# Kernel optimization log

Hardware: AMD Instinct MI355X
Metric: run time of the kernel (lower is better)

Reference implementation:

```python
import jax, jax.numpy as jnp
import numpy as np

PS = 16          # patch_size
E = 256          # embed_dim
NH = 4           # num_heads
THR = 1.5        # entropy_threshold (bits)
LN_EPS = 1e-5


def _ln(x, g, b):
    m = x.mean(-1, keepdims=True)
    v = ((x - m) ** 2).mean(-1, keepdims=True)
    return (x - m) / jnp.sqrt(v + LN_EPS) * g + b


def _forward(video, conv_w, conv_b, wq_w, wq_b, wk_w, wk_b, wv_w, wv_b,
             lnq_g, lnq_b, lnk_g, lnk_b, lnv_g, lnv_b,
             in_proj_w, in_proj_b, out_proj_w, out_proj_b,
             dense_w, dense_b, bproj_w, bproj_b, group_query, ent_table):
    # Conv3d(3->E, k=(3,PS,PS), s=(2,PS,PS), p=(1,0,0)) + ReLU
    x = jax.lax.conv_general_dilated(
        video, conv_w, window_strides=(2, PS, PS),
        padding=((1, 1), (0, 0), (0, 0)),
        dimension_numbers=('NCDHW', 'OIDHW', 'NCDHW'))
    x = jax.nn.relu(x + conv_b[None, :, None, None, None])
    B = x.shape[0]
    tokens = x.reshape(B, E, -1).transpose(0, 2, 1)  # [B, N, E]
    N = tokens.shape[1]

    # per-token byte (no_grad in torch)
    byte = jax.lax.stop_gradient(
        jnp.clip(jnp.round(tokens.mean(-1) * 255.0), 0, 255)).astype(jnp.int32)  # [B, N]
    # entropy predictor: probs = softmax(ent_table[last_byte]) (last byte of running seq)
    logits = ent_table[byte[0]]                      # [N, 256]
    p = jax.nn.softmax(logits, axis=-1)
    ent = -(p * jnp.log2(p + 1e-9)).sum(-1)          # [N]
    boundary = (ent > THR).astype(jnp.int32)
    seg = jnp.cumsum(boundary) - boundary            # exclusive cumsum -> segment id per token

    # DecoderCrossAttention with a single shared group_query per segment
    q0 = jnp.broadcast_to(group_query, (B, 1, E))    # byte_representations
    query = _ln(q0 @ wq_w.T + wq_b, lnq_g, lnq_b)    # [B,1,E]
    k = _ln(tokens @ wk_w.T + wk_b, lnk_g, lnk_b)    # [B,N,E]
    v = _ln(tokens @ wv_w.T + wv_b, lnv_g, lnv_b)

    Wqi, Wki, Wvi = in_proj_w[:E], in_proj_w[E:2 * E], in_proj_w[2 * E:]
    bqi, bki, bvi = in_proj_b[:E], in_proj_b[E:2 * E], in_proj_b[2 * E:]
    dh = E // NH
    qp = ((query @ Wqi.T + bqi) * (dh ** -0.5)).reshape(B, NH, dh)  # [B,H,dh]
    kp = (k @ Wki.T + bki).reshape(B, N, NH, dh)
    vp = (v @ Wvi.T + bvi).reshape(B, N, NH, dh)

    scores = jnp.einsum('bhd,bnhd->nbh', qp, kp)     # [N,B,H]
    smax = jax.ops.segment_max(scores, seg, num_segments=N)   # [N,B,H]
    w = jnp.exp(scores - smax[seg])
    denom = jax.ops.segment_sum(w, seg, num_segments=N)       # [N,B,H]
    num = jax.ops.segment_sum(w[..., None] * vp.transpose(1, 0, 2, 3),
                              seg, num_segments=N)            # [N,B,H,dh]
    count = jax.ops.segment_sum(jnp.ones((N,), scores.dtype), seg, num_segments=N)
    valid = count > 0
    safe = jnp.where(valid[:, None, None], denom, 1.0)
    attn = (num / safe[..., None]).transpose(1, 0, 2, 3).reshape(B, N, E)
    out = attn @ out_proj_w.T + out_proj_b
    out = out @ dense_w.T + dense_b
    out = out + q0                                   # residual with byte_representations
    patches = out @ bproj_w.T + bproj_b              # binary_proj
    return jnp.where(valid[None, :, None], patches, 0.0)  # [B, N, E] padded


def setup_inputs() -> dict:
    key = jax.random.key(0)
    ks = jax.random.split(key, 16)
    rn = lambda k, s, sc=0.02: jax.random.normal(k, s, jnp.float32) * sc
    z = lambda *s: jnp.zeros(s, jnp.float32)
    o = lambda *s: jnp.ones(s, jnp.float32)
    return {
        'video': jax.random.normal(ks[0], (4, 3, 32, 224, 224), jnp.float32),
        'conv_w': rn(ks[1], (E, 3, 3, PS, PS)), 'conv_b': z(E),
        'wq_w': rn(ks[2], (E, E)), 'wq_b': z(E),
        'wk_w': rn(ks[3], (E, E)), 'wk_b': z(E),
        'wv_w': rn(ks[4], (E, E)), 'wv_b': z(E),
        'lnq_g': o(E), 'lnq_b': z(E),
        'lnk_g': o(E), 'lnk_b': z(E),
        'lnv_g': o(E), 'lnv_b': z(E),
        'in_proj_w': rn(ks[5], (3 * E, E)), 'in_proj_b': z(3 * E),
        'out_proj_w': rn(ks[6], (E, E)), 'out_proj_b': z(E),
        'dense_w': rn(ks[7], (E, E)), 'dense_b': z(E),
        'bproj_w': rn(ks[8], (E, E)), 'bproj_b': z(E),
        'group_query': jax.random.normal(ks[9], (1, 1, E), jnp.float32),
        'ent_table': jax.random.normal(ks[10], (256, 256), jnp.float32) * 6.0,
    }


def reference(video, conv_w, conv_b, wq_w, wq_b, wk_w, wk_b, wv_w, wv_b,
              lnq_g, lnq_b, lnk_g, lnk_b, lnv_g, lnv_b,
              in_proj_w, in_proj_b, out_proj_w, out_proj_b,
              dense_w, dense_b, bproj_w, bproj_b, group_query, ent_table):
    return _forward(video, conv_w, conv_b, wq_w, wq_b, wk_w, wk_b, wv_w, wv_b,
                    lnq_g, lnq_b, lnk_g, lnk_b, lnv_g, lnv_b,
                    in_proj_w, in_proj_b, out_proj_w, out_proj_b,
                    dense_w, dense_b, bproj_w, bproj_b, group_query, ent_table)
```

## Files before the change

kernel.cpp:

```cpp
#include <hip/hip_runtime.h>
#include <hip/hip_bf16.h>
#include <math.h>

#define NTOK 3136
#define MT 12544
#define KCV 2304
#define THRESH 1.5f
#define LN_EPS 1e-5f

typedef short short8 __attribute__((ext_vector_type(8)));
typedef float f32x4 __attribute__((ext_vector_type(4)));
typedef float f32x16 __attribute__((ext_vector_type(16)));

__device__ __forceinline__ unsigned short f2bf(float f) {
    unsigned int u = __float_as_uint(f);
    u += 0x7fffu + ((u >> 16) & 1u);
    return (unsigned short)(u >> 16);
}
__device__ __forceinline__ float bf2f(unsigned short h) {
    return __uint_as_float(((unsigned int)h) << 16);
}
__device__ __forceinline__ unsigned int cvt_pk_bf16(float x0, float x1) {
    union { __hip_bfloat162 h; unsigned int u; } cv;
    cv.h = __float22bfloat162_rn(make_float2(x0, x1));
    return cv.u;
}
__device__ __forceinline__ void async16(const void* g, void* l) {
    __builtin_amdgcn_global_load_lds((const __attribute__((address_space(1))) void*)g,
                                     (__attribute__((address_space(3))) void*)l, 16, 0, 0);
}

__device__ __forceinline__ float wsum(float v) {
#pragma unroll
    for (int o = 32; o > 0; o >>= 1) v += __shfl_xor(v, o);
    return v;
}
__device__ __forceinline__ float wmax(float v) {
#pragma unroll
    for (int o = 32; o > 0; o >>= 1) v = fmaxf(v, __shfl_xor(v, o));
    return v;
}

__global__ __launch_bounds__(256) void prep_k(
    const float* __restrict__ cw, unsigned short* __restrict__ cwh,
    unsigned short* __restrict__ cwl,
    const float* __restrict__ s0, const float* __restrict__ s1, const float* __restrict__ s2,
    const float* __restrict__ s3, const float* __restrict__ s4, const float* __restrict__ s5,
    unsigned short* __restrict__ dst,
    const float* __restrict__ gq, const float* __restrict__ wq_w,
    const float* __restrict__ wq_b, const float* __restrict__ lnq_g,
    const float* __restrict__ lnq_b, const float* __restrict__ inW,
    const float* __restrict__ inB, float* __restrict__ qp)
{
    const int blk = blockIdx.x;
    if (blk < 288) {
        int i = blk * 256 + threadIdx.x;
        int e = i & 255, kg = i >> 8;
        const float4* sp = (const float4*)(cw + (size_t)e * KCV + kg * 8);
        float4 x0 = sp[0], x1 = sp[1];
        float av[8] = {x0.x, x0.y, x0.z, x0.w, x1.x, x1.y, x1.z, x1.w};
        short8 hh, ll;
#pragma unroll
        for (int j = 0; j < 8; ++j) {
            unsigned short h = f2bf(av[j]);
            hh[j] = (short)h;
            ll[j] = (short)f2bf(av[j] - bf2f(h));
        }
        size_t off = (size_t)kg * 2048 + e * 8;
        *(short8*)&cwh[off] = hh;
        *(short8*)&cwl[off] = ll;
    } else if (blk < 2336) {
        int i = (blk - 288) * 256 + threadIdx.x;
        if (i >= 524288) return;
        float v;
        if      (i <  65536) v = s0[i];
        else if (i < 131072) v = s1[i - 65536];
        else if (i < 327680) v = s2[i - 131072];
        else if (i < 393216) v = s3[i - 327680];
        else if (i < 458752) v = s4[i - 393216];
        else                 v = s5[i - 458752];
        dst[i] = f2bf(v);
    } else {
        __shared__ float sh[256];
        __shared__ float red[256];
        const int t = threadIdx.x;
        float acc = wq_b[t];
        for (int j = 0; j < 256; j++) acc += gq[j] * wq_w[t * 256 + j];
        red[t] = acc; __syncthreads();
        for (int o = 128; o > 0; o >>= 1) { if (t < o) red[t] += red[t + o]; __syncthreads(); }
        float m = red[0] * (1.f / 256.f);
        __syncthreads();
        float d = acc - m;
        red[t] = d * d; __syncthreads();
        for (int o = 128; o > 0; o >>= 1) { if (t < o) red[t] += red[t + o]; __syncthreads(); }
        float inv = 1.f / sqrtf(red[0] * (1.f / 256.f) + LN_EPS);
        sh[t] = d * inv * lnq_g[t] + lnq_b[t];
        __syncthreads();
        float a2 = inB[t];
        for (int j = 0; j < 256; j++) a2 += sh[j] * inW[t * 256 + j];
        qp[t] = a2 * 0.125f;
    }
}

__global__ __launch_bounds__(256, 3) void conv_mfma_k(
    const float* __restrict__ video, const unsigned short* __restrict__ cwh,
    const unsigned short* __restrict__ cwl, const float* __restrict__ cbias,
    float* __restrict__ tokmean8, unsigned short* __restrict__ outB)
{
    __shared__ __align__(16) unsigned short Bh[8192], Bl[8192];
    const int t    = threadIdx.x;
    const int lane = t & 63;
    const int w    = t >> 6;
    const int l31  = lane & 31, lh = lane >> 5;
    const int wr   = w >> 1,    wc = w & 1;
    const int v_  = blockIdx.x;
    const int s_  = (v_ & 7) * 98 + (v_ >> 3);
    const int mb  = s_ >> 2, eb = s_ & 3;
    const int m0  = mb * 64, e0 = eb * 64;

    const int m = m0 + wr * 32 + l31;
    const int b = m / NTOK, n = m % NTOK;
    const int d = n / 196, hw = n % 196;
    const int h = hw / 14, ww = hw % 14;
    const float* vb = video + (size_t)(b * 3) * (32 * 50176) + (h * 16) * 224 + ww * 16;
    const int dbase = 2 * d - 1;

    f32x16 acc = {};
    float4 a0, a1, a2, a3, a4, a5, a6, a7;
    float4 n0, n1, n2, n3, n4, n5, n6, n7;
    short8 rh0, rh1, rl0, rl1;

#define BLOAD(s)                                                                     \
    {                                                                                \
        const size_t g0 = (size_t)((s) * 8 + (t >> 5)) * 2048 + (e0 + (t & 31) * 2) * 8; \
        rh0 = *(const short8*)(cwh + g0);                                            \
        rh1 = *(const short8*)(cwh + g0 + 8);                                        \
        rl0 = *(const short8*)(cwl + g0);                                            \
        rl1 = *(const short8*)(cwl + g0 + 8);                                        \
    }
#define BSTORE(buf)                                                                  \
    {                                                                                \
        const int o = (buf) * 4096 + (t >> 5) * 512 + (t & 31) * 16;                 \
        *(short8*)&Bh[o]     = rh0;                                                  \
        *(short8*)&Bh[o + 8] = rh1;                                                  \
        *(short8*)&Bl[o]     = rl0;                                                  \
        *(short8*)&Bl[o + 8] = rl1;                                                  \
    }
#define LOAD_OCT(kv, x0, x1)                                                         \
    {                                                                                \
        const int k0  = (kv) + lh * 8;                                               \
        const int c   = k0 / 768;                                                    \
        const int rem = k0 - c * 768;                                                \
        const int kd  = rem >> 8;                                                    \
        const int r2  = rem & 255;                                                   \
        const int id  = dbase + kd;                                                  \
        x0 = make_float4(0.f, 0.f, 0.f, 0.f); x1 = x0;                               \
        if (id >= 0) {                                                               \
            const float* p = vb + (size_t)c * (32 * 50176) + id * 50176 +            \
                             (r2 >> 4) * 224 + (r2 & 15);                            \
            x0 = *(const float4*)p;                                                  \
            x1 = *(const float4*)(p + 4);                                            \
        }                                                                            \
    }
#define CVT_AB(y0, y1, fah, fal)                                                     \
    short8 fah, fal;                                                                 \
    {                                                                                \
        float av[8] = {y0.x, y0.y, y0.z, y0.w, y1.x, y1.y, y1.z, y1.w};              \
        unsigned int ph[4], pl[4];                                                   \
        _Pragma("unroll")                                                            \
        for (int j = 0; j < 4; ++j) {                                                \
            float u0 = av[2 * j], u1 = av[2 * j + 1];                                \
            unsigned int hu = cvt_pk_bf16(u0, u1);                                   \
            float r0 = u0 - __uint_as_float(hu << 16);                               \
            float r1 = u1 - __uint_as_float(hu & 0xffff0000u);                       \
            ph[j] = hu;                                                              \
            pl[j] = cvt_pk_bf16(r0, r1);                                             \
        }                                                                            \
        int4 phv = make_int4(ph[0], ph[1], ph[2], ph[3]);                            \
        int4 plv = make_int4(pl[0], pl[1], pl[2], pl[3]);                            \
        fah = *(short8*)&phv;                                                        \
        fal = *(short8*)&plv;                                                        \
    }
#define KCHUNK(i, ya, yb, cbuf)                                                      \
    {                                                                                \
        CVT_AB(ya, yb, fah, fal);                                                    \
        const int rb = (cbuf) * 4096 + ((2 * (i) + lh) * 64 + wc * 32 + l31) * 8;    \
        short8 fbh = *(const short8*)&Bh[rb];                                        \
        short8 fbl = *(const short8*)&Bl[rb];                                        \
        acc = __builtin_amdgcn_mfma_f32_32x32x16_bf16(fah, fbh, acc, 0, 0, 0);       \
        acc = __builtin_amdgcn_mfma_f32_32x32x16_bf16(fah, fbl, acc, 0, 0, 0);       \
        acc = __builtin_amdgcn_mfma_f32_32x32x16_bf16(fal, fbh, acc, 0, 0, 0);       \
    }

    BLOAD(0);
    LOAD_OCT(0,  a0, a1);
    LOAD_OCT(16, a2, a3);
    LOAD_OCT(32, a4, a5);
    LOAD_OCT(48, a6, a7);
    BSTORE(0);
    __syncthreads();

    for (int s = 0; s < 36; ++s) {
        const int cbuf = s & 1;
        if (s + 1 < 36) {
            BLOAD(s + 1);
            const int kb = (s + 1) * 64;
            LOAD_OCT(kb,      n0, n1);
            LOAD_OCT(kb + 16, n2, n3);
            LOAD_OCT(kb + 32, n4, n5);
            LOAD_OCT(kb + 48, n6, n7);
        }
        KCHUNK(0, a0, a1, cbuf);
        KCHUNK(1, a2, a3, cbuf);
        KCHUNK(2, a4, a5, cbuf);
        KCHUNK(3, a6, a7, cbuf);
        if (s + 1 < 36) BSTORE(cbuf ^ 1);
        __syncthreads();
        a0 = n0; a1 = n1; a2 = n2; a3 = n3;
        a4 = n4; a5 = n5; a6 = n6; a7 = n7;
    }
#undef BLOAD
#undef BSTORE
#undef LOAD_OCT
#undef CVT_AB
#undef KCHUNK

    const int e = e0 + wc * 32 + l31;
    const float bias = cbias[e];
    const bool emit_tm = (m0 < NTOK);
#pragma unroll
    for (int r = 0; r < 16; ++r) {
        int row = (r & 3) + 8 * (r >> 2) + 4 * lh;
        int mm  = m0 + wr * 32 + row;
        float vv = fmaxf(acc[r] + bias, 0.f);
        outB[(size_t)mm * 256 + e] = f2bf(vv);
        float sv = vv;
        sv += __shfl_xor(sv, 1); sv += __shfl_xor(sv, 2);
        sv += __shfl_xor(sv, 4); sv += __shfl_xor(sv, 8);
        sv += __shfl_xor(sv, 16);
        if (emit_tm && l31 == 0)
            tokmean8[(size_t)(eb * 2 + wc) * NTOK + mm] = sv;
    }
}

__global__ __launch_bounds__(256) void gemm_single_k(
    const unsigned short* __restrict__ A, const unsigned short* __restrict__ W,
    const float* __restrict__ bias, const float* __restrict__ addvec,
    const int* __restrict__ Sptr, float* __restrict__ outF, unsigned short* __restrict__ outB)
{
    __shared__ __align__(16) unsigned short As[8192], Bs[8192];
    const int t = threadIdx.x, lane = t & 63, w = t >> 6;
    const int v_ = blockIdx.x;
    const int s_ = (v_ & 7) * 98 + (v_ >> 3);
    const int m0 = (s_ >> 2) * 64, e0 = (s_ & 3) * 64;
    const int l15 = lane & 15, lq = lane >> 4;
    const unsigned short* ga = A + (size_t)(m0 + lane) * 256;
    const unsigned short* gb = W + (size_t)(e0 + lane) * 256;
#pragma unroll
    for (int kg = w; kg < 16; kg += 4) {
        async16(ga + kg * 8, &As[kg * 512]);
        async16(gb + kg * 8, &Bs[kg * 512]);
    }
    f32x4 acc[4] = {};
    __syncthreads();
#pragma unroll
    for (int s = 0; s < 4; ++s) {
        int kg = s * 4 + lq;
        short8 a = *(const short8*)&As[kg * 512 + (w * 16 + l15) * 8];
#pragma unroll
        for (int ct = 0; ct < 4; ++ct) {
            short8 bb = *(const short8*)&Bs[kg * 512 + (ct * 16 + l15) * 8];
            acc[ct] = __builtin_amdgcn_mfma_f32_16x16x32_bf16(a, bb, acc[ct], 0, 0, 0);
        }
    }
    __syncthreads();
#pragma unroll
    for (int kg = w; kg < 16; kg += 4) {
        async16(ga + (16 + kg) * 8, &As[kg * 512]);
        async16(gb + (16 + kg) * 8, &Bs[kg * 512]);
    }
    __syncthreads();
#pragma unroll
    for (int s = 0; s < 4; ++s) {
        int kg = s * 4 + lq;
        short8 a = *(const short8*)&As[kg * 512 + (w * 16 + l15) * 8];
#pragma unroll
        for (int ct = 0; ct < 4; ++ct) {
            short8 bb = *(const short8*)&Bs[kg * 512 + (ct * 16 + l15) * 8];
            acc[ct] = __builtin_amdgcn_mfma_f32_16x16x32_bf16(a, bb, acc[ct], 0, 0, 0);
        }
    }
    int S = Sptr ? *Sptr : 0x7fffffff;
    int rbase = m0 + w * 16 + lq * 4;
#pragma unroll
    for (int ct = 0; ct < 4; ++ct) {
        int e = e0 + ct * 16 + l15;
        float bv = bias[e] + (addvec ? addvec[e] : 0.f);
#pragma unroll
        for (int r = 0; r < 4; ++r) {
            int mm = rbase + r;
            float vv = acc[ct][r] + bv;
            if ((mm % NTOK) >= S) vv = 0.f;
            size_t off = (size_t)mm * 256 + e;
            if (outF) outF[off] = vv;
            if (outB) outB[off] = f2bf(vv);
        }
    }
}

__global__ __launch_bounds__(256) void gemm_dual_k(
    const unsigned short* __restrict__ A0, const unsigned short* __restrict__ A1,
    const unsigned short* __restrict__ W,
    const float* __restrict__ bias0, const float* __restrict__ bias1,
    unsigned short* __restrict__ outB0, unsigned short* __restrict__ outB1,
    const float* __restrict__ qp, float* __restrict__ sc)
{
    __shared__ __align__(16) unsigned short As[8192], Bs[8192];
    const int t = threadIdx.x, lane = t & 63, w = t >> 6;
    const int v_ = blockIdx.x;
    const int s_ = (v_ & 7) * 196 + (v_ >> 3);
    const int mb = s_ >> 3, ebg = s_ & 7;
    const int half = ebg >> 2;
    const unsigned short* A = half ? A1 : A0;
    const float* bias = half ? bias1 : bias0;
    unsigned short* outB = half ? outB1 : outB0;
    const int m0 = mb * 64, eg0 = ebg * 64, el0 = (ebg & 3) * 64;
    const int l15 = lane & 15, lq = lane >> 4;
    const unsigned short* ga = A + (size_t)(m0 + lane) * 256;
    const unsigned short* gb = W + (size_t)(eg0 + lane) * 256;
#pragma unroll
    for (int kg = w; kg < 16; kg += 4) {
        async16(ga + kg * 8, &As[kg * 512]);
        async16(gb + kg * 8, &Bs[kg * 512]);
    }
    f32x4 acc[4] = {};
    __syncthreads();
#pragma unroll
    for (int s = 0; s < 4; ++s) {
        int kg = s * 4 + lq;
        short8 a = *(const short8*)&As[kg * 512 + (w * 16 + l15) * 8];
#pragma unroll
        for (int ct = 0; ct < 4; ++ct) {
            short8 bb = *(const short8*)&Bs[kg * 512 + (ct * 16 + l15) * 8];
            acc[ct] = __builtin_amdgcn_mfma_f32_16x16x32_bf16(a, bb, acc[ct], 0, 0, 0);
        }
    }
    __syncthreads();
#pragma unroll
    for (int kg = w; kg < 16; kg += 4) {
        async16(ga + (16 + kg) * 8, &As[kg * 512]);
        async16(gb + (16 + kg) * 8, &Bs[kg * 512]);
    }
    __syncthreads();
#pragma unroll
    for (int s = 0; s < 4; ++s) {
        int kg = s * 4 + lq;
        short8 a = *(const short8*)&As[kg * 512 + (w * 16 + l15) * 8];
#pragma unroll
        for (int ct = 0; ct < 4; ++ct) {
            short8 bb = *(const short8*)&Bs[kg * 512 + (ct * 16 + l15) * 8];
            acc[ct] = __builtin_amdgcn_mfma_f32_16x16x32_bf16(a, bb, acc[ct], 0, 0, 0);
        }
    }
    int rbase = m0 + w * 16 + lq * 4;
    if (qp && half == 0) {
        float sp[4] = {0.f, 0.f, 0.f, 0.f};
#pragma unroll
        for (int ct = 0; ct < 4; ++ct) {
            int e = el0 + ct * 16 + l15;
            float bv = bias[e];
            float qv = qp[e];
#pragma unroll
            for (int r = 0; r < 4; ++r) sp[r] += (acc[ct][r] + bv) * qv;
        }
#pragma unroll
        for (int r = 0; r < 4; ++r) {
            sp[r] += __shfl_xor(sp[r], 1); sp[r] += __shfl_xor(sp[r], 2);
            sp[r] += __shfl_xor(sp[r], 4); sp[r] += __shfl_xor(sp[r], 8);
        }
        if (l15 == 0) {
#pragma unroll
            for (int r = 0; r < 4; ++r) {
                int mm = rbase + r;
                int bb = mm / NTOK, nn = mm % NTOK;
                sc[(bb * 4 + ebg) * NTOK + nn] = sp[r];
            }
        }
    } else {
#pragma unroll
        for (int ct = 0; ct < 4; ++ct) {
            int e = el0 + ct * 16 + l15;
            float bv = bias[e];
#pragma unroll
            for (int r = 0; r < 4; ++r) {
                float vv = acc[ct][r] + bv;
                outB[(size_t)(rbase + r) * 256 + e] = f2bf(vv);
            }
        }
    }
}

__global__ __launch_bounds__(256) void boundary_k(
    const float* __restrict__ tokmean8, const float* __restrict__ ent_table,
    int* __restrict__ boundary)
{
    int n    = blockIdx.x * 4 + (threadIdx.x >> 6);
    int lane = threadIdx.x & 63;
    float s0 = tokmean8[n];
    float s1 = tokmean8[NTOK + n];
    float s2 = tokmean8[2 * NTOK + n];
    float s3 = tokmean8[3 * NTOK + n];
    float s4 = tokmean8[4 * NTOK + n];
    float s5 = tokmean8[5 * NTOK + n];
    float s6 = tokmean8[6 * NTOK + n];
    float s7 = tokmean8[7 * NTOK + n];
    float mean = (((s0 + s1) + (s2 + s3)) + ((s4 + s5) + (s6 + s7))) * (1.f / 256.f);
    float bf = rintf(mean * 255.f);
    bf = fminf(fmaxf(bf, 0.f), 255.f);
    int byte = (int)bf;
    const float4 lg = reinterpret_cast<const float4*>(ent_table + byte * 256)[lane];
    float mx = wmax(fmaxf(fmaxf(lg.x, lg.y), fmaxf(lg.z, lg.w)));
    float e0 = expf(lg.x - mx), e1 = expf(lg.y - mx), e2 = expf(lg.z - mx), e3 = expf(lg.w - mx);
    float z = wsum(e0 + e1 + e2 + e3);
    float iz = 1.f / z;
    float p0 = e0 * iz, p1 = e1 * iz, p2 = e2 * iz, p3 = e3 * iz;
    float ep = -(p0 * log2f(p0 + 1e-9f) + p1 * log2f(p1 + 1e-9f) +
                 p2 * log2f(p2 + 1e-9f) + p3 * log2f(p3 + 1e-9f));
    ep = wsum(ep);
    if (lane == 0) boundary[n] = (ep > THRESH) ? 1 : 0;
}

__global__ __launch_bounds__(256) void scan_k(const int* __restrict__ boundary,
    int* __restrict__ seg_start, int* __restrict__ Sptr)
{
    __shared__ int sums[256];
    const int t = threadIdx.x;
    const int CH = 13;
    int base = t * CH;
    int s = 0;
    for (int i = 0; i < CH; i++) { int n = base + i; if (n < NTOK) s += boundary[n]; }
    sums[t] = s; __syncthreads();
    for (int o = 1; o < 256; o <<= 1) {
        int v = sums[t];
        int u = (t >= o) ? sums[t - o] : 0;
        __syncthreads();
        sums[t] = v + u;
        __syncthreads();
    }
    int run = (t == 0) ? 0 : sums[t - 1];
    if (t == 0) seg_start[0] = 0;
    for (int i = 0; i < CH; i++) {
        int n = base + i;
        if (n >= NTOK) break;
        int v = boundary[n];
        if (n == NTOK - 1) { Sptr[0] = run + 1; seg_start[run + 1] = NTOK; }
        if (v && (n + 1 < NTOK)) seg_start[run + 1] = n + 1;
        run += v;
    }
}

__global__ __launch_bounds__(256) void lnKV_k(
    const unsigned short* __restrict__ Pk, const unsigned short* __restrict__ Pv,
    const float* __restrict__ gk, const float* __restrict__ bk,
    const float* __restrict__ gv, const float* __restrict__ bv,
    unsigned short* __restrict__ Yk, unsigned short* __restrict__ Yv)
{
    int row  = blockIdx.x * 4 + (threadIdx.x >> 6);
    int lane = threadIdx.x & 63;
    int half = row >= MT;
    int r    = half ? row - MT : row;
    const unsigned short* X = half ? Pv : Pk;
    const float* g = half ? gv : gk;
    const float* b = half ? bv : bk;
    unsigned short* Y = half ? Yv : Yk;
    ushort4 xr = reinterpret_cast<const ushort4*>(X + (size_t)r * 256)[lane];
    float x0 = bf2f(xr.x), x1 = bf2f(xr.y), x2 = bf2f(xr.z), x3 = bf2f(xr.w);
    float m = wsum(x0 + x1 + x2 + x3) * (1.f / 256.f);
    float d0 = x0 - m, d1 = x1 - m, d2 = x2 - m, d3 = x3 - m;
    float var = wsum(d0 * d0 + d1 * d1 + d2 * d2 + d3 * d3) * (1.f / 256.f);
    float inv = 1.f / sqrtf(var + LN_EPS);
    float4 g4 = reinterpret_cast<const float4*>(g)[lane];
    float4 b4 = reinterpret_cast<const float4*>(b)[lane];
    ushort4 y;
    y.x = f2bf(d0 * inv * g4.x + b4.x);
    y.y = f2bf(d1 * inv * g4.y + b4.y);
    y.z = f2bf(d2 * inv * g4.z + b4.z);
    y.w = f2bf(d3 * inv * g4.w + b4.w);
    reinterpret_cast<ushort4*>(Y + (size_t)r * 256)[lane] = y;
}

__global__ __launch_bounds__(256) void attn_bf_k(const float* __restrict__ sc,
    const unsigned short* __restrict__ vp, const int* __restrict__ seg_start,
    const int* __restrict__ Sptr, unsigned short* __restrict__ attn)
{
    int s    = blockIdx.x;
    int b    = blockIdx.y;
    int h    = threadIdx.x >> 6;
    int lane = threadIdx.x & 63;
    unsigned short* orow = attn + ((size_t)b * NTOK + s) * 256;
    int S = *Sptr;
    if (s >= S) { orow[h * 64 + lane] = 0; return; }
    int st = seg_start[s], en = seg_start[s + 1];
    const float* scr = sc + (b * 4 + h) * NTOK;
    float m = -1e30f;
    for (int n = st; n < en; n++) m = fmaxf(m, scr[n]);
    float den = 0.f, acc = 0.f;
    const unsigned short* vpb = vp + (size_t)b * NTOK * 256 + h * 64 + lane;
    for (int n = st; n < en; n++) {
        float wgt = expf(scr[n] - m);
        den += wgt;
        acc += wgt * bf2f(vpb[(size_t)n * 256]);
    }
    orow[h * 64 + lane] = f2bf(acc / den);
}

extern "C" void kernel_launch(void* const* d_in, const int* in_sizes, int n_in,
                              void* d_out, int out_size, void* d_ws, size_t ws_size,
                              hipStream_t stream)
{
    const float* video      = (const float*)d_in[0];
    const float* conv_w     = (const float*)d_in[1];
    const float* conv_b     = (const float*)d_in[2];
    const float* wq_w       = (const float*)d_in[3];
    const float* wq_b       = (const float*)d_in[4];
    const float* wk_w       = (const float*)d_in[5];
    const float* wk_b       = (const float*)d_in[6];
    const float* wv_w       = (const float*)d_in[7];
    const float* wv_b       = (const float*)d_in[8];
    const float* lnq_g      = (const float*)d_in[9];
    const float* lnq_b      = (const float*)d_in[10];
    const float* lnk_g      = (const float*)d_in[11];
    const float* lnk_b      = (const float*)d_in[12];
    const float* lnv_g      = (const float*)d_in[13];
    const float* lnv_b      = (const float*)d_in[14];
    const float* in_proj_w  = (const float*)d_in[15];
    const float* in_proj_b  = (const float*)d_in[16];
    const float* out_proj_w = (const float*)d_in[17];
    const float* out_proj_b = (const float*)d_in[18];
    const float* dense_w    = (const float*)d_in[19];
    const float* dense_b    = (const float*)d_in[20];
    const float* bproj_w    = (const float*)d_in[21];
    const float* bproj_b    = (const float*)d_in[22];
    const float* group_q    = (const float*)d_in[23];
    const float* ent_table  = (const float*)d_in[24];
    float* out = (float*)d_out;

    float* tokmean8 = (float*)d_ws;
    unsigned short* Pk  = (unsigned short*)(tokmean8 + 32768);
    unsigned short* Pv  = Pk  + (size_t)MT * 256;
    unsigned short* B1  = Pv  + (size_t)MT * 256;
    unsigned short* B2k = B1  + (size_t)MT * 256;
    unsigned short* B2v = B2k + (size_t)MT * 256;
    unsigned short* B3v = B2v + (size_t)MT * 256;
    unsigned short* cwh = B3v + (size_t)MT * 256;
    unsigned short* cwl = cwh + 256 * KCV;
    unsigned short* wpool = cwl + 256 * KCV;
    float* sc = (float*)(wpool + 524288);
    float* qp = sc + 16 * NTOK;
    int* boundary  = (int*)(qp + 256);
    int* seg_start = boundary + NTOK;
    int* Sp        = seg_start + (NTOK + 1);

    const unsigned short* inpb   = wpool + 131072;
    const unsigned short* outpb  = wpool + 327680;
    const unsigned short* denseb = wpool + 393216;
    const unsigned short* bprojb = wpool + 458752;

    dim3 blk(256);
    prep_k<<<dim3(2337), blk, 0, stream>>>(conv_w, cwh, cwl,
                                           wk_w, wv_w, in_proj_w, out_proj_w,
                                           dense_w, bproj_w, wpool,
                                           group_q, wq_w, wq_b, lnq_g, lnq_b,
                                           in_proj_w, in_proj_b, qp);
    conv_mfma_k<<<dim3(784), blk, 0, stream>>>(video, cwh, cwl, conv_b, tokmean8, B1);
    boundary_k<<<dim3(NTOK / 4), blk, 0, stream>>>(tokmean8, ent_table, boundary);
    scan_k<<<dim3(1), blk, 0, stream>>>(boundary, seg_start, Sp);
    gemm_dual_k<<<dim3(1568), blk, 0, stream>>>(B1, B1, wpool, wk_b, wv_b, Pk, Pv,
                                                nullptr, nullptr);
    lnKV_k<<<dim3(2 * MT / 4), blk, 0, stream>>>(Pk, Pv, lnk_g, lnk_b, lnv_g, lnv_b,
                                                 B2k, B2v);
    gemm_dual_k<<<dim3(1568), blk, 0, stream>>>(B2k, B2v, inpb + 65536,
                                                in_proj_b + 256, in_proj_b + 512,
                                                nullptr, B3v, qp, sc);
    attn_bf_k<<<dim3(NTOK, 4), blk, 0, stream>>>(sc, B3v, seg_start, Sp, B1);
    gemm_single_k<<<dim3(784), blk, 0, stream>>>(B1, outpb, out_proj_b,
                                                 nullptr, nullptr, nullptr, B2k);
    gemm_single_k<<<dim3(784), blk, 0, stream>>>(B2k, denseb, dense_b,
                                                 group_q, nullptr, nullptr, B2v);
    gemm_single_k<<<dim3(784), blk, 0, stream>>>(B2v, bprojb, bproj_b,
                                                 nullptr, Sp, out, nullptr);
}
```

Measured before the change: 361.9 us.

## Retile conv MFMA kernel to 128x32 blocks with split accumulators

The conv implicit-GEMM block tile changes from 64x64 with 2x2 waves to 128 rows x 32 channels, with each wave owning 32 distinct rows, so the shared-memory weight tile is halved. The three-MFMA error-compensated chain now splits into two accumulators to break the serial dependency between MFMAs. The trade-off is that each video patch element is loaded by twice as many blocks (8 channel groups instead of 4), increasing global/L2 traffic on the A side, while B traffic per block falls. The tokmean bound check is now done per row.

```diff
diff --git a/kernel.cpp b/kernel.cpp
--- a/kernel.cpp
+++ b/kernel.cpp
@@ -107,44 +107,39 @@
     const unsigned short* __restrict__ cwl, const float* __restrict__ cbias,
     float* __restrict__ tokmean8, unsigned short* __restrict__ outB)
 {
-    __shared__ __align__(16) unsigned short Bh[8192], Bl[8192];
+    __shared__ __align__(16) unsigned short Bh[4096], Bl[4096];
     const int t    = threadIdx.x;
     const int lane = t & 63;
     const int w    = t >> 6;
     const int l31  = lane & 31, lh = lane >> 5;
-    const int wr   = w >> 1,    wc = w & 1;
     const int v_  = blockIdx.x;
     const int s_  = (v_ & 7) * 98 + (v_ >> 3);
-    const int mb  = s_ >> 2, eb = s_ & 3;
-    const int m0  = mb * 64, e0 = eb * 64;
-
-    const int m = m0 + wr * 32 + l31;
+    const int mb  = s_ >> 3, ebg = s_ & 7;
+    const int m0  = mb * 128, e0 = ebg * 32;
+
+    const int m = m0 + w * 32 + l31;
     const int b = m / NTOK, n = m % NTOK;
     const int d = n / 196, hw = n % 196;
     const int h = hw / 14, ww = hw % 14;
     const float* vb = video + (size_t)(b * 3) * (32 * 50176) + (h * 16) * 224 + ww * 16;
     const int dbase = 2 * d - 1;
 
-    f32x16 acc = {};
+    f32x16 accA = {}, accB = {};
     float4 a0, a1, a2, a3, a4, a5, a6, a7;
     float4 n0, n1, n2, n3, n4, n5, n6, n7;
-    short8 rh0, rh1, rl0, rl1;
+    short8 rh0, rl0;
 
 #define BLOAD(s)                                                                     \
     {                                                                                \
-        const size_t g0 = (size_t)((s) * 8 + (t >> 5)) * 2048 + (e0 + (t & 31) * 2) * 8; \
+        const size_t g0 = (size_t)((s) * 8 + (t >> 5)) * 2048 + (e0 + (t & 31)) * 8; \
         rh0 = *(const short8*)(cwh + g0);                                            \
-        rh1 = *(const short8*)(cwh + g0 + 8);                                        \
         rl0 = *(const short8*)(cwl + g0);                                            \
-        rl1 = *(const short8*)(cwl + g0 + 8);                                        \
     }
 #define BSTORE(buf)                                                                  \
     {                                                                                \
-        const int o = (buf) * 4096 + (t >> 5) * 512 + (t & 31) * 16;                 \
-        *(short8*)&Bh[o]     = rh0;                                                  \
-        *(short8*)&Bh[o + 8] = rh1;                                                  \
-        *(short8*)&Bl[o]     = rl0;                                                  \
-        *(short8*)&Bl[o + 8] = rl1;                                                  \
+        const int o = (buf) * 2048 + (t >> 5) * 256 + (t & 31) * 8;                  \
+        *(short8*)&Bh[o] = rh0;                                                      \
+        *(short8*)&Bl[o] = rl0;                                                      \
     }
 #define LOAD_OCT(kv, x0, x1)                                                         \
     {                                                                                \
@@ -184,12 +179,12 @@
 #define KCHUNK(i, ya, yb, cbuf)                                                      \
     {                                                                                \
         CVT_AB(ya, yb, fah, fal);                                                    \
-        const int rb = (cbuf) * 4096 + ((2 * (i) + lh) * 64 + wc * 32 + l31) * 8;    \
+        const int rb = (cbuf) * 2048 + (2 * (i) + lh) * 256 + l31 * 8;               \
         short8 fbh = *(const short8*)&Bh[rb];                                        \
         short8 fbl = *(const short8*)&Bl[rb];                                        \
-        acc = __builtin_amdgcn_mfma_f32_32x32x16_bf16(fah, fbh, acc, 0, 0, 0);       \
-        acc = __builtin_amdgcn_mfma_f32_32x32x16_bf16(fah, fbl, acc, 0, 0, 0);       \
-        acc = __builtin_amdgcn_mfma_f32_32x32x16_bf16(fal, fbh, acc, 0, 0, 0);       \
+        accA = __builtin_amdgcn_mfma_f32_32x32x16_bf16(fah, fbh, accA, 0, 0, 0);     \
+        accB = __builtin_amdgcn_mfma_f32_32x32x16_bf16(fah, fbl, accB, 0, 0, 0);     \
+        accA = __builtin_amdgcn_mfma_f32_32x32x16_bf16(fal, fbh, accA, 0, 0, 0);     \
     }
 
     BLOAD(0);
@@ -225,21 +220,20 @@
 #undef CVT_AB
 #undef KCHUNK
 
-    const int e = e0 + wc * 32 + l31;
+    const int e = e0 + l31;
     const float bias = cbias[e];
-    const bool emit_tm = (m0 < NTOK);
 #pragma unroll
     for (int r = 0; r < 16; ++r) {
         int row = (r & 3) + 8 * (r >> 2) + 4 * lh;
-        int mm  = m0 + wr * 32 + row;
-        float vv = fmaxf(acc[r] + bias, 0.f);
+        int mm  = m0 + w * 32 + row;
+        float vv = fmaxf(accA[r] + accB[r] + bias, 0.f);
         outB[(size_t)mm * 256 + e] = f2bf(vv);
         float sv = vv;
         sv += __shfl_xor(sv, 1); sv += __shfl_xor(sv, 2);
         sv += __shfl_xor(sv, 4); sv += __shfl_xor(sv, 8);
         sv += __shfl_xor(sv, 16);
-        if (emit_tm && l31 == 0)
-            tokmean8[(size_t)(eb * 2 + wc) * NTOK + mm] = sv;
+        if (l31 == 0 && mm < NTOK)
+            tokmean8[(size_t)ebg * NTOK + mm] = sv;
     }
 }
 
```

Result: no change. 359.3 us (-0.7%).

## Fuse K/V LayerNorm into in-proj GEMM and split conv K across waves

Applied to the files above, without the earlier changes.

The separate LayerNorm kernel over K and V projections is removed. Its row statistics and normalization are now computed inside a new GEMM kernel that loads full 256-wide rows into LDS, normalizes them on the fly, and feeds the in_proj MFMA, which drops a full round trip of the intermediate activations. The conv kernel is also reorganized so that waves split the K dimension and each wave computes two N tiles with separate accumulators. The partial sums are then reduced through LDS, which raises MFMA independence at the cost of extra LDS traffic and a sync. LN stats now use E[x^2]-mean^2 in a single pass, which is slightly less numerically stable.

```diff
diff --git a/kernel.cpp b/kernel.cpp
--- a/kernel.cpp
+++ b/kernel.cpp
@@ -112,39 +112,39 @@
     const int lane = t & 63;
     const int w    = t >> 6;
     const int l31  = lane & 31, lh = lane >> 5;
-    const int wr   = w >> 1,    wc = w & 1;
+    const int wm   = w & 1, wk = w >> 1;
     const int v_  = blockIdx.x;
     const int s_  = (v_ & 7) * 98 + (v_ >> 3);
-    const int mb  = s_ >> 2, eb = s_ & 3;
-    const int m0  = mb * 64, e0 = eb * 64;
-
-    const int m = m0 + wr * 32 + l31;
+    const int mb  = s_ >> 2, ebi = s_ & 3;
+    const int m0  = mb * 64, e0 = ebi * 64;
+
+    const int m = m0 + wm * 32 + l31;
     const int b = m / NTOK, n = m % NTOK;
     const int d = n / 196, hw = n % 196;
     const int h = hw / 14, ww = hw % 14;
     const float* vb = video + (size_t)(b * 3) * (32 * 50176) + (h * 16) * 224 + ww * 16;
     const int dbase = 2 * d - 1;
 
-    f32x16 acc = {};
-    float4 a0, a1, a2, a3, a4, a5, a6, a7;
-    float4 n0, n1, n2, n3, n4, n5, n6, n7;
+    f32x16 accA0 = {}, accB0 = {}, accA1 = {}, accB1 = {};
+    float4 a0, a1, a2, a3;
+    float4 n0 = {}, n1 = {}, n2 = {}, n3 = {};
     short8 rh0, rh1, rl0, rl1;
 
 #define BLOAD(s)                                                                     \
     {                                                                                \
-        const size_t g0 = (size_t)((s) * 8 + (t >> 5)) * 2048 + (e0 + (t & 31) * 2) * 8; \
+        const size_t g0 = (size_t)((s) * 8 + 2 * w) * 2048 + (e0 + lane) * 8;        \
         rh0 = *(const short8*)(cwh + g0);                                            \
-        rh1 = *(const short8*)(cwh + g0 + 8);                                        \
+        rh1 = *(const short8*)(cwh + g0 + 2048);                                     \
         rl0 = *(const short8*)(cwl + g0);                                            \
-        rl1 = *(const short8*)(cwl + g0 + 8);                                        \
+        rl1 = *(const short8*)(cwl + g0 + 2048);                                     \
     }
 #define BSTORE(buf)                                                                  \
     {                                                                                \
-        const int o = (buf) * 4096 + (t >> 5) * 512 + (t & 31) * 16;                 \
-        *(short8*)&Bh[o]     = rh0;                                                  \
-        *(short8*)&Bh[o + 8] = rh1;                                                  \
-        *(short8*)&Bl[o]     = rl0;                                                  \
-        *(short8*)&Bl[o + 8] = rl1;                                                  \
+        const int o = (buf) * 4096 + 2 * w * 512 + lane * 8;                         \
+        *(short8*)&Bh[o]       = rh0;                                                \
+        *(short8*)&Bh[o + 512] = rh1;                                                \
+        *(short8*)&Bl[o]       = rl0;                                                \
+        *(short8*)&Bl[o + 512] = rl1;                                                \
     }
 #define LOAD_OCT(kv, x0, x1)                                                         \
     {                                                                                \
@@ -181,22 +181,25 @@
         fah = *(short8*)&phv;                                                        \
         fal = *(short8*)&plv;                                                        \
     }
-#define KCHUNK(i, ya, yb, cbuf)                                                      \
+#define KCHUNK(kc, ya, yb, cbuf)                                                     \
     {                                                                                \
         CVT_AB(ya, yb, fah, fal);                                                    \
-        const int rb = (cbuf) * 4096 + ((2 * (i) + lh) * 64 + wc * 32 + l31) * 8;    \
-        short8 fbh = *(const short8*)&Bh[rb];                                        \
-        short8 fbl = *(const short8*)&Bl[rb];                                        \
-        acc = __builtin_amdgcn_mfma_f32_32x32x16_bf16(fah, fbh, acc, 0, 0, 0);       \
-        acc = __builtin_amdgcn_mfma_f32_32x32x16_bf16(fah, fbl, acc, 0, 0, 0);       \
-        acc = __builtin_amdgcn_mfma_f32_32x32x16_bf16(fal, fbh, acc, 0, 0, 0);       \
+        const int rb0 = (cbuf) * 4096 + (wk * 4 + (kc) * 2 + lh) * 512 + l31 * 8;    \
+        short8 fbh0 = *(const short8*)&Bh[rb0];                                      \
+        short8 fbl0 = *(const short8*)&Bl[rb0];                                      \
+        short8 fbh1 = *(const short8*)&Bh[rb0 + 256];                                \
+        short8 fbl1 = *(const short8*)&Bl[rb0 + 256];                                \
+        accA0 = __builtin_amdgcn_mfma_f32_32x32x16_bf16(fah, fbh0, accA0, 0, 0, 0);  \
+        accB0 = __builtin_amdgcn_mfma_f32_32x32x16_bf16(fah, fbl0, accB0, 0, 0, 0);  \
+        accA1 = __builtin_amdgcn_mfma_f32_32x32x16_bf16(fah, fbh1, accA1, 0, 0, 0);  \
+        accB1 = __builtin_amdgcn_mfma_f32_32x32x16_bf16(fah, fbl1, accB1, 0, 0, 0);  \
+        accA0 = __builtin_amdgcn_mfma_f32_32x32x16_bf16(fal, fbh0, accA0, 0, 0, 0);  \
+        accA1 = __builtin_amdgcn_mfma_f32_32x32x16_bf16(fal, fbh1, accA1, 0, 0, 0);  \
     }
 
     BLOAD(0);
-    LOAD_OCT(0,  a0, a1);
-    LOAD_OCT(16, a2, a3);
-    LOAD_OCT(32, a4, a5);
-    LOAD_OCT(48, a6, a7);
+    LOAD_OCT(wk * 32,      a0, a1);
+    LOAD_OCT(wk * 32 + 16, a2, a3);
     BSTORE(0);
     __syncthreads();
 
@@ -204,20 +207,15 @@
         const int cbuf = s & 1;
         if (s + 1 < 36) {
             BLOAD(s + 1);
-            const int kb = (s + 1) * 64;
+            const int kb = (s + 1) * 64 + wk * 32;
             LOAD_OCT(kb,      n0, n1);
             LOAD_OCT(kb + 16, n2, n3);
-            LOAD_OCT(kb + 32, n4, n5);
-            LOAD_OCT(kb + 48, n6, n7);
         }
         KCHUNK(0, a0, a1, cbuf);
         KCHUNK(1, a2, a3, cbuf);
-        KCHUNK(2, a4, a5, cbuf);
-        KCHUNK(3, a6, a7, cbuf);
         if (s + 1 < 36) BSTORE(cbuf ^ 1);
         __syncthreads();
         a0 = n0; a1 = n1; a2 = n2; a3 = n3;
-        a4 = n4; a5 = n5; a6 = n6; a7 = n7;
     }
 #undef BLOAD
 #undef BSTORE
@@ -225,21 +223,39 @@
 #undef CVT_AB
 #undef KCHUNK
 
-    const int e = e0 + wc * 32 + l31;
-    const float bias = cbias[e];
-    const bool emit_tm = (m0 < NTOK);
-#pragma unroll
-    for (int r = 0; r < 16; ++r) {
-        int row = (r & 3) + 8 * (r >> 2) + 4 * lh;
-        int mm  = m0 + wr * 32 + row;
-        float vv = fmaxf(acc[r] + bias, 0.f);
-        outB[(size_t)mm * 256 + e] = f2bf(vv);
-        float sv = vv;
-        sv += __shfl_xor(sv, 1); sv += __shfl_xor(sv, 2);
-        sv += __shfl_xor(sv, 4); sv += __shfl_xor(sv, 8);
-        sv += __shfl_xor(sv, 16);
-        if (emit_tm && l31 == 0)
-            tokmean8[(size_t)(eb * 2 + wc) * NTOK + mm] = sv;
+    f32x16 p0, p1;
+#pragma unroll
+    for (int r = 0; r < 16; ++r) { p0[r] = accA0[r] + accB0[r]; p1[r] = accA1[r] + accB1[r]; }
+    float* scr = (float*)Bh;
+    if (wk == 1) {
+#pragma unroll
+        for (int r = 0; r < 16; ++r) {
+            scr[r * 256 + (wm * 2 + 0) * 64 + lane] = p0[r];
+            scr[r * 256 + (wm * 2 + 1) * 64 + lane] = p1[r];
+        }
+    }
+    __syncthreads();
+    if (wk == 0) {
+        const bool emit_tm = (m0 < NTOK);
+#pragma unroll
+        for (int ti = 0; ti < 2; ++ti) {
+            const int e = e0 + ti * 32 + l31;
+            const float bias = cbias[e];
+#pragma unroll
+            for (int r = 0; r < 16; ++r) {
+                float pv = (ti == 0 ? p0[r] : p1[r]) + scr[r * 256 + (wm * 2 + ti) * 64 + lane];
+                int row = (r & 3) + 8 * (r >> 2) + 4 * lh;
+                int mm  = m0 + wm * 32 + row;
+                float vv = fmaxf(pv + bias, 0.f);
+                outB[(size_t)mm * 256 + e] = f2bf(vv);
+                float sv = vv;
+                sv += __shfl_xor(sv, 1); sv += __shfl_xor(sv, 2);
+                sv += __shfl_xor(sv, 4); sv += __shfl_xor(sv, 8);
+                sv += __shfl_xor(sv, 16);
+                if (emit_tm && l31 == 0)
+                    tokmean8[(size_t)(ebi * 2 + ti) * NTOK + mm] = sv;
+            }
+        }
     }
 }
 
@@ -312,8 +328,7 @@
     const unsigned short* __restrict__ A0, const unsigned short* __restrict__ A1,
     const unsigned short* __restrict__ W,
     const float* __restrict__ bias0, const float* __restrict__ bias1,
-    unsigned short* __restrict__ outB0, unsigned short* __restrict__ outB1,
-    const float* __restrict__ qp, float* __restrict__ sc)
+    unsigned short* __restrict__ outB0, unsigned short* __restrict__ outB1)
 {
     __shared__ __align__(16) unsigned short As[8192], Bs[8192];
     const int t = threadIdx.x, lane = t & 63, w = t >> 6;
@@ -363,7 +378,104 @@
         }
     }
     int rbase = m0 + w * 16 + lq * 4;
-    if (qp && half == 0) {
+#pragma unroll
+    for (int ct = 0; ct < 4; ++ct) {
+        int e = el0 + ct * 16 + l15;
+        float bv = bias[e];
+#pragma unroll
+        for (int r = 0; r < 4; ++r) {
+            float vv = acc[ct][r] + bv;
+            outB[(size_t)(rbase + r) * 256 + e] = f2bf(vv);
+        }
+    }
+}
+
+__global__ __launch_bounds__(256, 2) void gemm_ln_k(
+    const unsigned short* __restrict__ A0, const unsigned short* __restrict__ A1,
+    const unsigned short* __restrict__ W,
+    const float* __restrict__ bias0, const float* __restrict__ bias1,
+    const float* __restrict__ g0, const float* __restrict__ b0,
+    const float* __restrict__ g1, const float* __restrict__ b1,
+    unsigned short* __restrict__ outVp, const float* __restrict__ qp,
+    float* __restrict__ sc)
+{
+    __shared__ __align__(16) unsigned short As[16384], Bs[16384];
+    __shared__ float pst[2][4][64];
+    __shared__ float rmean[64], rinv[64];
+    const int t = threadIdx.x, lane = t & 63, w = t >> 6;
+    const int v_ = blockIdx.x;
+    const int s_ = (v_ & 7) * 196 + (v_ >> 3);
+    const int mb = s_ >> 3, ebg = s_ & 7;
+    const int half = ebg >> 2;
+    const unsigned short* A = half ? A1 : A0;
+    const float* bias = half ? bias1 : bias0;
+    const float* lng  = half ? g1 : g0;
+    const float* lnb  = half ? b1 : b0;
+    const int m0 = mb * 64, eg0 = ebg * 64, el0 = (ebg & 3) * 64;
+    const int l15 = lane & 15, lq = lane >> 4;
+    const unsigned short* ga = A + (size_t)(m0 + lane) * 256;
+    const unsigned short* gb = W + (size_t)(eg0 + lane) * 256;
+#pragma unroll
+    for (int kg = w; kg < 32; kg += 4) {
+        async16(ga + kg * 8, &As[kg * 512]);
+        async16(gb + kg * 8, &Bs[kg * 512]);
+    }
+    __syncthreads();
+    {
+        float sum = 0.f, sq = 0.f;
+#pragma unroll
+        for (int k8 = 0; k8 < 8; ++k8) {
+            short8 x = *(const short8*)&As[(w * 8 + k8) * 512 + lane * 8];
+#pragma unroll
+            for (int j = 0; j < 8; ++j) {
+                float xv = bf2f((unsigned short)x[j]);
+                sum += xv; sq += xv * xv;
+            }
+        }
+        pst[0][w][lane] = sum; pst[1][w][lane] = sq;
+    }
+    __syncthreads();
+    if (w == 0) {
+        float s4 = (pst[0][0][lane] + pst[0][1][lane]) + (pst[0][2][lane] + pst[0][3][lane]);
+        float q4 = (pst[1][0][lane] + pst[1][1][lane]) + (pst[1][2][lane] + pst[1][3][lane]);
+        float mean = s4 * (1.f / 256.f);
+        float var  = q4 * (1.f / 256.f) - mean * mean;
+        rmean[lane] = mean;
+        rinv[lane]  = 1.f / sqrtf(var + LN_EPS);
+    }
+    __syncthreads();
+    const float myMean = rmean[w * 16 + l15];
+    const float myInv  = rinv [w * 16 + l15];
+
+    f32x4 acc[4] = {};
+#pragma unroll
+    for (int s = 0; s < 8; ++s) {
+        int kg = s * 4 + lq;
+        short8 araw = *(const short8*)&As[kg * 512 + (w * 16 + l15) * 8];
+        float4 gA = *(const float4*)&lng[kg * 8];
+        float4 gB = *(const float4*)&lng[kg * 8 + 4];
+        float4 bA = *(const float4*)&lnb[kg * 8];
+        float4 bB = *(const float4*)&lnb[kg * 8 + 4];
+        float y[8];
+        y[0] = (bf2f((unsigned short)araw[0]) - myMean) * myInv * gA.x + bA.x;
+        y[1] = (bf2f((unsigned short)araw[1]) - myMean) * myInv * gA.y + bA.y;
+        y[2] = (bf2f((unsigned short)araw[2]) - myMean) * myInv * gA.z + bA.z;
+        y[3] = (bf2f((unsigned short)araw[3]) - myMean) * myInv * gA.w + bA.w;
+        y[4] = (bf2f((unsigned short)araw[4]) - myMean) * myInv * gB.x + bB.x;
+        y[5] = (bf2f((unsigned short)araw[5]) - myMean) * myInv * gB.y + bB.y;
+        y[6] = (bf2f((unsigned short)araw[6]) - myMean) * myInv * gB.z + bB.z;
+        y[7] = (bf2f((unsigned short)araw[7]) - myMean) * myInv * gB.w + bB.w;
+        int4 pk = make_int4(cvt_pk_bf16(y[0], y[1]), cvt_pk_bf16(y[2], y[3]),
+                            cvt_pk_bf16(y[4], y[5]), cvt_pk_bf16(y[6], y[7]));
+        short8 a = *(short8*)&pk;
+#pragma unroll
+        for (int ct = 0; ct < 4; ++ct) {
+            short8 bb = *(const short8*)&Bs[kg * 512 + (ct * 16 + l15) * 8];
+            acc[ct] = __builtin_amdgcn_mfma_f32_16x16x32_bf16(a, bb, acc[ct], 0, 0, 0);
+        }
+    }
+    int rbase = m0 + w * 16 + lq * 4;
+    if (half == 0) {
         float sp[4] = {0.f, 0.f, 0.f, 0.f};
 #pragma unroll
         for (int ct = 0; ct < 4; ++ct) {
@@ -394,7 +506,7 @@
 #pragma unroll
             for (int r = 0; r < 4; ++r) {
                 float vv = acc[ct][r] + bv;
-                outB[(size_t)(rbase + r) * 256 + e] = f2bf(vv);
+                outVp[(size_t)(rbase + r) * 256 + e] = f2bf(vv);
             }
         }
     }
@@ -457,36 +569,6 @@
         if (v && (n + 1 < NTOK)) seg_start[run + 1] = n + 1;
         run += v;
     }
-}
-
-__global__ __launch_bounds__(256) void lnKV_k(
-    const unsigned short* __restrict__ Pk, const unsigned short* __restrict__ Pv,
-    const float* __restrict__ gk, const float* __restrict__ bk,
-    const float* __restrict__ gv, const float* __restrict__ bv,
-    unsigned short* __restrict__ Yk, unsigned short* __restrict__ Yv)
-{
-    int row  = blockIdx.x * 4 + (threadIdx.x >> 6);
-    int lane = threadIdx.x & 63;
-    int half = row >= MT;
-    int r    = half ? row - MT : row;
-    const unsigned short* X = half ? Pv : Pk;
-    const float* g = half ? gv : gk;
-    const float* b = half ? bv : bk;
-    unsigned short* Y = half ? Yv : Yk;
-    ushort4 xr = reinterpret_cast<const ushort4*>(X + (size_t)r * 256)[lane];
-    float x0 = bf2f(xr.x), x1 = bf2f(xr.y), x2 = bf2f(xr.z), x3 = bf2f(xr.w);
-    float m = wsum(x0 + x1 + x2 + x3) * (1.f / 256.f);
-    float d0 = x0 - m, d1 = x1 - m, d2 = x2 - m, d3 = x3 - m;
-    float var = wsum(d0 * d0 + d1 * d1 + d2 * d2 + d3 * d3) * (1.f / 256.f);
-    float inv = 1.f / sqrtf(var + LN_EPS);
-    float4 g4 = reinterpret_cast<const float4*>(g)[lane];
-    float4 b4 = reinterpret_cast<const float4*>(b)[lane];
-    ushort4 y;
-    y.x = f2bf(d0 * inv * g4.x + b4.x);
-    y.y = f2bf(d1 * inv * g4.y + b4.y);
-    y.z = f2bf(d2 * inv * g4.z + b4.z);
-    y.w = f2bf(d3 * inv * g4.w + b4.w);
-    reinterpret_cast<ushort4*>(Y + (size_t)r * 256)[lane] = y;
 }
 
 __global__ __launch_bounds__(256) void attn_bf_k(const float* __restrict__ sc,
@@ -575,13 +657,11 @@
     conv_mfma_k<<<dim3(784), blk, 0, stream>>>(video, cwh, cwl, conv_b, tokmean8, B1);
     boundary_k<<<dim3(NTOK / 4), blk, 0, stream>>>(tokmean8, ent_table, boundary);
     scan_k<<<dim3(1), blk, 0, stream>>>(boundary, seg_start, Sp);
-    gemm_dual_k<<<dim3(1568), blk, 0, stream>>>(B1, B1, wpool, wk_b, wv_b, Pk, Pv,
-                                                nullptr, nullptr);
-    lnKV_k<<<dim3(2 * MT / 4), blk, 0, stream>>>(Pk, Pv, lnk_g, lnk_b, lnv_g, lnv_b,
-                                                 B2k, B2v);
-    gemm_dual_k<<<dim3(1568), blk, 0, stream>>>(B2k, B2v, inpb + 65536,
-                                                in_proj_b + 256, in_proj_b + 512,
-                                                nullptr, B3v, qp, sc);
+    gemm_dual_k<<<dim3(1568), blk, 0, stream>>>(B1, B1, wpool, wk_b, wv_b, Pk, Pv);
+    gemm_ln_k<<<dim3(1568), blk, 0, stream>>>(Pk, Pv, inpb + 65536,
+                                              in_proj_b + 256, in_proj_b + 512,
+                                              lnk_g, lnk_b, lnv_g, lnv_b,
+                                              B3v, qp, sc);
     attn_bf_k<<<dim3(NTOK, 4), blk, 0, stream>>>(sc, B3v, seg_start, Sp, B1);
     gemm_single_k<<<dim3(784), blk, 0, stream>>>(B1, outpb, out_proj_b,
                                                  nullptr, nullptr, nullptr, B2k);
```

Result: faster. 348.5 us (-3.7%).
